# Kernel tuning notes

Hardware: AMD Instinct MI355X
Metric: run time of the kernel (lower is better)

The kernel has to match this reference:

```python
import jax, jax.numpy as jnp
import numpy as np

L, B, T = 512, 1024, 48

def setup_inputs() -> dict:
    key = jax.random.key(0)
    k0, k1, k2, k3, k4 = jax.random.split(key, 5)
    emissions = jax.random.normal(k0, (L, B, T), dtype=jnp.float32)
    tags = jax.random.randint(k1, (L, B), 0, T)
    mask = jnp.ones((L, B), dtype=jnp.int32)
    start_transitions = 0.1 * jax.random.normal(k2, (T,), dtype=jnp.float32)
    end_transitions = 0.1 * jax.random.normal(k3, (T,), dtype=jnp.float32)
    transitions = 0.1 * jax.random.normal(k4, (T, T), dtype=jnp.float32)
    return {"emissions": emissions, "tags": tags, "mask": mask,
            "start_transitions": start_transitions,
            "end_transitions": end_transitions,
            "transitions": transitions}


def _crf_llh(emissions, tags, mask, start_transitions, end_transitions, transitions):
    seq_len, batch, num_tags = emissions.shape
    maskf = mask.astype(emissions.dtype)

    # ---- numerator: joint log-likelihood of the gold tag path ----
    # emission score of the gold tag at each position: (L, B)
    emis_at_tags = jnp.take_along_axis(emissions, tags[:, :, None], axis=2)[:, :, 0]
    llh = start_transitions[tags[0]]                                  # (B,)
    llh = llh + jnp.sum(emis_at_tags[:-1] * maskf[:-1], axis=0)       # emissions for t=0..L-2
    trans_scores = transitions[tags[:-1], tags[1:]]                   # (L-1, B)
    llh = llh + jnp.sum(trans_scores * maskf[1:], axis=0)
    last_idx = jnp.sum(mask, axis=0).astype(jnp.int32) - 1            # (B,)
    last_tags = tags[last_idx, jnp.arange(batch)]                     # (B,)
    llh = llh + end_transitions[last_tags]
    llh = llh + emissions[-1][jnp.arange(batch), last_tags] * maskf[-1]

    # ---- denominator: log partition function via log-sum-exp scan ----
    def step(log_prob, x):
        e_t, m_t = x  # (B, T), (B,)
        # score[b, j] = logsumexp_i( log_prob[b, i] + trans[i, j] ) + e_t[b, j]
        score = jax.nn.logsumexp(log_prob[:, :, None] + transitions[None, :, :], axis=1) + e_t
        log_prob = jnp.where(m_t[:, None] > 0, score, log_prob)
        return log_prob, None

    init = start_transitions[None, :] + emissions[0]                  # (B, T)
    log_prob, _ = jax.lax.scan(step, init, (emissions[1:], maskf[1:]))
    log_z = jax.nn.logsumexp(log_prob + end_transitions[None, :], axis=1)  # (B,)

    return jnp.sum(llh - log_z)  # summed=True


def reference(emissions, tags, mask, start_transitions, end_transitions, transitions):
    return _crf_llh(emissions, tags, mask, start_transitions, end_transitions, transitions)
```

## Files before the change

kernel.cpp:

```cpp
#include <hip/hip_runtime.h>

#define Lq 512
#define Bn 1024
#define Tq 48

typedef float f32x4 __attribute__((ext_vector_type(4)));
typedef short s16x8 __attribute__((ext_vector_type(8)));
typedef unsigned u32x4 __attribute__((ext_vector_type(4)));

#define MFMA(a, b, c) __builtin_amdgcn_mfma_f32_16x16x32_bf16((a), (b), (c), 0, 0, 0)
#define SB __builtin_amdgcn_sched_barrier(0)

__device__ __forceinline__ unsigned cvtpk(float lo, float hi) {
    unsigned r;
    asm("v_cvt_pk_bf16_f32 %0, %1, %2" : "=v"(r) : "v"(lo), "v"(hi));
    return r;
}
__device__ __forceinline__ short f2b(float x) {
    unsigned u = __float_as_uint(x);
    return (short)((u + 0x7fffu + ((u >> 16) & 1u)) >> 16);
}

#define PACKB do {                                                            \
    unsigned d0_ = cvtpk(pn0[0], pn0[1]), d1_ = cvtpk(pn0[2], pn0[3]);        \
    unsigned d2_ = cvtpk(pn1[0], pn1[1]), d3_ = cvtpk(pn1[2], pn1[3]);        \
    unsigned d4_ = cvtpk(pn2[0], pn2[1]), d5_ = cvtpk(pn2[2], pn2[3]);        \
    u32x4 b0_ = {d0_, d1_, d2_, d3_};                                         \
    u32x4 b1_ = {d4_, d5_, 0u, 0u};                                           \
    Bk0 = __builtin_bit_cast(s16x8, b0_);                                     \
    Bk1 = __builtin_bit_cast(s16x8, b1_);                                     \
} while (0)

#define STEP(EA, EB, EC, MV, RS) do {                                         \
    f32x4 C0_ = MFMA(aw00, Bk0, Zf); f32x4 D0_ = MFMA(aw01, Bk1, Zf);         \
    f32x4 C1_ = MFMA(aw10, Bk0, Zf); f32x4 D1_ = MFMA(aw11, Bk1, Zf);         \
    f32x4 C2_ = MFMA(aw20, Bk0, Zf); f32x4 D2_ = MFMA(aw21, Bk1, Zf);         \
    pn0[0] = (MV) ? (C0_[0] + D0_[0]) * __expf((EA)[0]) : pn0[0];             \
    pn0[1] = (MV) ? (C0_[1] + D0_[1]) * __expf((EA)[1]) : pn0[1];             \
    pn0[2] = (MV) ? (C0_[2] + D0_[2]) * __expf((EA)[2]) : pn0[2];             \
    pn0[3] = (MV) ? (C0_[3] + D0_[3]) * __expf((EA)[3]) : pn0[3];             \
    pn1[0] = (MV) ? (C1_[0] + D1_[0]) * __expf((EB)[0]) : pn1[0];             \
    pn1[1] = (MV) ? (C1_[1] + D1_[1]) * __expf((EB)[1]) : pn1[1];             \
    pn1[2] = (MV) ? (C1_[2] + D1_[2]) * __expf((EB)[2]) : pn1[2];             \
    pn1[3] = (MV) ? (C1_[3] + D1_[3]) * __expf((EB)[3]) : pn1[3];             \
    pn2[0] = (MV) ? (C2_[0] + D2_[0]) * __expf((EC)[0]) : pn2[0];             \
    pn2[1] = (MV) ? (C2_[1] + D2_[1]) * __expf((EC)[1]) : pn2[1];             \
    pn2[2] = (MV) ? (C2_[2] + D2_[2]) * __expf((EC)[2]) : pn2[2];             \
    pn2[3] = (MV) ? (C2_[3] + D2_[3]) * __expf((EC)[3]) : pn2[3];             \
    if (RS) {                                                                 \
        float rep_ = __shfl(pn0[0], cidx, 64);         \
        int k_ = ((__float_as_int(rep_) >> 23) & 0xff) - 126;                 \
        float scl_ = __int_as_float((127 - k_) << 23);        \
        pn0[0]*=scl_; pn0[1]*=scl_; pn0[2]*=scl_; pn0[3]*=scl_;               \
        pn1[0]*=scl_; pn1[1]*=scl_; pn1[2]*=scl_; pn1[3]*=scl_;               \
        pn2[0]*=scl_; pn2[1]*=scl_; pn2[2]*=scl_; pn2[3]*=scl_;               \
        c2 += k_;                                                             \
    }                                                                         \
    PACKB;                                                                    \
} while (0)

#define LOAD_SLOT(D, T) do {                                                  \
    int t_ = (T); vf_##D = (t_ < Lq); int tc_ = vf_##D ? t_ : (Lq - 1);       \
    const float* ep_ = em + ((size_t)tc_ * Bn + bidx) * Tq + 4 * qidx;        \
    const int*   mp_ = mask + tc_ * Bn + bidx;                                \
    asm volatile("global_load_dwordx4 %0, %1, off" : "=v"(ea_##D) : "v"(ep_));      \
    asm volatile("global_load_dwordx4 %0, %1, off" : "=v"(eb_##D) : "v"(ep_ + 16)); \
    asm volatile("global_load_dwordx4 %0, %1, off" : "=v"(ec_##D) : "v"(ep_ + 32)); \
    asm volatile("global_load_dword %0, %1, off"   : "=v"(mv_##D) : "v"(mp_));      \
} while (0)

#define WAITP do { asm volatile("s_waitcnt vmcnt(12)"); SB; } while (0)

__global__ __launch_bounds__(64, 1) void crf_fused(
    const float* __restrict__ em, const int* __restrict__ tags,
    const int* __restrict__ mask, const float* __restrict__ startT,
    const float* __restrict__ endT, const float* __restrict__ trans,
    float* __restrict__ out)
{
    const int j = threadIdx.x;
    __shared__ float shf[Tq * Tq];

    if (blockIdx.x < 64) {
        const int cidx = j & 15;
        const int qidx = j >> 4;
        const int bidx = blockIdx.x * 16 + cidx;

        for (int i = j; i < Tq * Tq; i += 64) shf[i] = trans[i];
        __syncthreads();
        s16x8 aw00, aw01, aw10, aw11, aw20, aw21;
#pragma unroll
        for (int i = 0; i < 8; ++i) {
            int l0 = (i < 4) ? (4 * qidx + i) : (12 + 4 * qidx + i);
            aw00[i] = f2b(__expf(shf[l0 * Tq + cidx]));
            aw10[i] = f2b(__expf(shf[l0 * Tq + 16 + cidx]));
            aw20[i] = f2b(__expf(shf[l0 * Tq + 32 + cidx]));
            if (i < 4) {
                int l1 = 32 + 4 * qidx + i;
                aw01[i] = f2b(__expf(shf[l1 * Tq + cidx]));
                aw11[i] = f2b(__expf(shf[l1 * Tq + 16 + cidx]));
                aw21[i] = f2b(__expf(shf[l1 * Tq + 32 + cidx]));
            } else {
                aw01[i] = 0; aw11[i] = 0; aw21[i] = 0;
            }
        }

        f32x4 pn0, pn1, pn2;
        {
            const float* e0p = em + (size_t)bidx * Tq;
            f32x4 ea = *(const f32x4*)(e0p + 4 * qidx);
            f32x4 eb = *(const f32x4*)(e0p + 16 + 4 * qidx);
            f32x4 ec = *(const f32x4*)(e0p + 32 + 4 * qidx);
#pragma unroll
            for (int i = 0; i < 4; ++i) {
                pn0[i] = __expf(startT[ 0 + 4 * qidx + i] + ea[i]);
                pn1[i] = __expf(startT[16 + 4 * qidx + i] + eb[i]);
                pn2[i] = __expf(startT[32 + 4 * qidx + i] + ec[i]);
            }
        }

        const f32x4 Zf = {0.f, 0.f, 0.f, 0.f};
        s16x8 Bk0, Bk1;
        int c2 = 0;
        PACKB;

        f32x4 ea_0, eb_0, ec_0, ea_1, eb_1, ec_1;
        f32x4 ea_2, eb_2, ec_2, ea_3, eb_3, ec_3;
        int mv_0, mv_1, mv_2, mv_3;
        int vf_0, vf_1, vf_2, vf_3;

        asm volatile("s_waitcnt vmcnt(0)");
        LOAD_SLOT(0, 1); LOAD_SLOT(1, 2); LOAD_SLOT(2, 3); LOAD_SLOT(3, 4);

        for (int ch = 0; ch < 128; ++ch) {
            const int tb = 1 + 4 * ch;
            WAITP; STEP(ea_0, eb_0, ec_0, (mv_0 & vf_0), 0); LOAD_SLOT(0, tb + 4);
            WAITP; STEP(ea_1, eb_1, ec_1, (mv_1 & vf_1), 0); LOAD_SLOT(1, tb + 5);
            WAITP; STEP(ea_2, eb_2, ec_2, (mv_2 & vf_2), 0); LOAD_SLOT(2, tb + 6);
            WAITP; STEP(ea_3, eb_3, ec_3, (mv_3 & vf_3), 1); LOAD_SLOT(3, tb + 7);
        }

        float zacc = 0.f;
#pragma unroll
        for (int i = 0; i < 4; ++i) {
            zacc += pn0[i] * __expf(endT[ 0 + 4 * qidx + i]);
            zacc += pn1[i] * __expf(endT[16 + 4 * qidx + i]);
            zacc += pn2[i] * __expf(endT[32 + 4 * qidx + i]);
        }
        zacc += __shfl_xor(zacc, 16, 64);
        zacc += __shfl_xor(zacc, 32, 64);
        float nl = -(__logf(zacc) + (float)c2 * 0.6931471805599453f);
        nl += __shfl_xor(nl, 1, 64);
        nl += __shfl_xor(nl, 2, 64);
        nl += __shfl_xor(nl, 4, 64);
        nl += __shfl_xor(nl, 8, 64);
        if (j == 0) atomicAdd(out, nl);
        asm volatile("s_waitcnt vmcnt(0)");
    } else {
        const int bid = blockIdx.x - 64;
        float c = 0.0f;
        for (int id = bid * 64 + j; id < Lq * Bn; id += 512 * 64) {
            int t  = id >> 10;
            int bb = id & (Bn - 1);
            int tag = tags[id];
            int m_t = mask[id];
            if (t == 0) c += startT[tag];
            bool is_last;
            if (t < Lq - 1) {
                if (m_t) c += em[(size_t)id * Tq + tag];
                int tag1 = tags[id + Bn];
                int m1   = mask[id + Bn];
                if (m1) c += trans[tag * Tq + tag1];
                is_last = (m_t != 0) && (m1 == 0);
            } else {
                is_last = (m_t != 0);
            }
            if (is_last) {
                c += endT[tag];
                int mL = mask[(Lq - 1) * Bn + bb];
                if (mL) c += em[((size_t)(Lq - 1) * Bn + bb) * Tq + tag];
            }
        }
#pragma unroll
        for (int off = 32; off >= 1; off >>= 1)
            c += __shfl_xor(c, off, 64);
        if (j == 0) atomicAdd(out, c);
    }
}

extern "C" void kernel_launch(void* const* d_in, const int* in_sizes, int n_in,
                              void* d_out, int out_size, void* d_ws, size_t ws_size,
                              hipStream_t stream) {
    const float* em     = (const float*)d_in[0];
    const int*   tags   = (const int*)d_in[1];
    const int*   mask   = (const int*)d_in[2];
    const float* startT = (const float*)d_in[3];
    const float* endT   = (const float*)d_in[4];
    const float* trans  = (const float*)d_in[5];
    float* out = (float*)d_out;

    hipMemsetAsync(out, 0, sizeof(float), stream);
    crf_fused<<<576, 64, 0, stream>>>(em, tags, mask, startT, endT, trans, out);
}
```

Measured before the change: 150.6 us.

## Interleave two independent batch chains per wave to hide recurrence latency

Each forward-recursion wave now processes two 16-column batch groups (A and B) in an interleaved fashion, halving the recursion block count from 64 to 32. It also accumulates the two MFMA halves in place of separate adds, precomputes exp of emissions one slot ahead, and hoists the rescale exponent read before the rescale step. The intent is to fill the serial MFMA→exp→pack dependency chain with independent work from the second chain. In exchange, register pressure grows and fewer CUs are active for the latency-bound scan.

```diff
diff --git a/kernel.cpp b/kernel.cpp
--- a/kernel.cpp
+++ b/kernel.cpp
@@ -21,55 +21,73 @@
     return (short)((u + 0x7fffu + ((u >> 16) & 1u)) >> 16);
 }
 
-#define PACKB do {                                                            \
-    unsigned d0_ = cvtpk(pn0[0], pn0[1]), d1_ = cvtpk(pn0[2], pn0[3]);        \
-    unsigned d2_ = cvtpk(pn1[0], pn1[1]), d3_ = cvtpk(pn1[2], pn1[3]);        \
-    unsigned d4_ = cvtpk(pn2[0], pn2[1]), d5_ = cvtpk(pn2[2], pn2[3]);        \
+#define PACKBX(S) do {                                                        \
+    unsigned d0_ = cvtpk(pn##S##0[0], pn##S##0[1]);                           \
+    unsigned d1_ = cvtpk(pn##S##0[2], pn##S##0[3]);                           \
+    unsigned d2_ = cvtpk(pn##S##1[0], pn##S##1[1]);                           \
+    unsigned d3_ = cvtpk(pn##S##1[2], pn##S##1[3]);                           \
+    unsigned d4_ = cvtpk(pn##S##2[0], pn##S##2[1]);                           \
+    unsigned d5_ = cvtpk(pn##S##2[2], pn##S##2[3]);                           \
     u32x4 b0_ = {d0_, d1_, d2_, d3_};                                         \
     u32x4 b1_ = {d4_, d5_, 0u, 0u};                                           \
-    Bk0 = __builtin_bit_cast(s16x8, b0_);                                     \
-    Bk1 = __builtin_bit_cast(s16x8, b1_);                                     \
-} while (0)
-
-#define STEP(EA, EB, EC, MV, RS) do {                                         \
-    f32x4 C0_ = MFMA(aw00, Bk0, Zf); f32x4 D0_ = MFMA(aw01, Bk1, Zf);         \
-    f32x4 C1_ = MFMA(aw10, Bk0, Zf); f32x4 D1_ = MFMA(aw11, Bk1, Zf);         \
-    f32x4 C2_ = MFMA(aw20, Bk0, Zf); f32x4 D2_ = MFMA(aw21, Bk1, Zf);         \
-    pn0[0] = (MV) ? (C0_[0] + D0_[0]) * __expf((EA)[0]) : pn0[0];             \
-    pn0[1] = (MV) ? (C0_[1] + D0_[1]) * __expf((EA)[1]) : pn0[1];             \
-    pn0[2] = (MV) ? (C0_[2] + D0_[2]) * __expf((EA)[2]) : pn0[2];             \
-    pn0[3] = (MV) ? (C0_[3] + D0_[3]) * __expf((EA)[3]) : pn0[3];             \
-    pn1[0] = (MV) ? (C1_[0] + D1_[0]) * __expf((EB)[0]) : pn1[0];             \
-    pn1[1] = (MV) ? (C1_[1] + D1_[1]) * __expf((EB)[1]) : pn1[1];             \
-    pn1[2] = (MV) ? (C1_[2] + D1_[2]) * __expf((EB)[2]) : pn1[2];             \
-    pn1[3] = (MV) ? (C1_[3] + D1_[3]) * __expf((EB)[3]) : pn1[3];             \
-    pn2[0] = (MV) ? (C2_[0] + D2_[0]) * __expf((EC)[0]) : pn2[0];             \
-    pn2[1] = (MV) ? (C2_[1] + D2_[1]) * __expf((EC)[1]) : pn2[1];             \
-    pn2[2] = (MV) ? (C2_[2] + D2_[2]) * __expf((EC)[2]) : pn2[2];             \
-    pn2[3] = (MV) ? (C2_[3] + D2_[3]) * __expf((EC)[3]) : pn2[3];             \
+    Bk##S##0 = __builtin_bit_cast(s16x8, b0_);                                \
+    Bk##S##1 = __builtin_bit_cast(s16x8, b1_);                                \
+} while (0)
+
+#define STEPX(S, EA, EB, EC, MV, RS) do {                                     \
+    f32x4 C0_ = MFMA(aw00, Bk##S##0, Zf); C0_ = MFMA(aw01, Bk##S##1, C0_);    \
+    f32x4 C1_ = MFMA(aw10, Bk##S##0, Zf); C1_ = MFMA(aw11, Bk##S##1, C1_);    \
+    f32x4 C2_ = MFMA(aw20, Bk##S##0, Zf); C2_ = MFMA(aw21, Bk##S##1, C2_);    \
+    pn##S##0[0] = (MV) ? C0_[0] * (EA)[0] : pn##S##0[0];                      \
+    pn##S##0[1] = (MV) ? C0_[1] * (EA)[1] : pn##S##0[1];                      \
+    pn##S##0[2] = (MV) ? C0_[2] * (EA)[2] : pn##S##0[2];                      \
+    pn##S##0[3] = (MV) ? C0_[3] * (EA)[3] : pn##S##0[3];                      \
+    pn##S##1[0] = (MV) ? C1_[0] * (EB)[0] : pn##S##1[0];                      \
+    pn##S##1[1] = (MV) ? C1_[1] * (EB)[1] : pn##S##1[1];                      \
+    pn##S##1[2] = (MV) ? C1_[2] * (EB)[2] : pn##S##1[2];                      \
+    pn##S##1[3] = (MV) ? C1_[3] * (EB)[3] : pn##S##1[3];                      \
+    pn##S##2[0] = (MV) ? C2_[0] * (EC)[0] : pn##S##2[0];                      \
+    pn##S##2[1] = (MV) ? C2_[1] * (EC)[1] : pn##S##2[1];                      \
+    pn##S##2[2] = (MV) ? C2_[2] * (EC)[2] : pn##S##2[2];                      \
+    pn##S##2[3] = (MV) ? C2_[3] * (EC)[3] : pn##S##2[3];                      \
     if (RS) {                                                                 \
-        float rep_ = __shfl(pn0[0], cidx, 64);         \
-        int k_ = ((__float_as_int(rep_) >> 23) & 0xff) - 126;                 \
-        float scl_ = __int_as_float((127 - k_) << 23);        \
-        pn0[0]*=scl_; pn0[1]*=scl_; pn0[2]*=scl_; pn0[3]*=scl_;               \
-        pn1[0]*=scl_; pn1[1]*=scl_; pn1[2]*=scl_; pn1[3]*=scl_;               \
-        pn2[0]*=scl_; pn2[1]*=scl_; pn2[2]*=scl_; pn2[3]*=scl_;               \
-        c2 += k_;                                                             \
+        pn##S##0[0]*=scl##S; pn##S##0[1]*=scl##S;                             \
+        pn##S##0[2]*=scl##S; pn##S##0[3]*=scl##S;                             \
+        pn##S##1[0]*=scl##S; pn##S##1[1]*=scl##S;                             \
+        pn##S##1[2]*=scl##S; pn##S##1[3]*=scl##S;                             \
+        pn##S##2[0]*=scl##S; pn##S##2[1]*=scl##S;                             \
+        pn##S##2[2]*=scl##S; pn##S##2[3]*=scl##S;                             \
+        c2##S += k##S;                                                        \
     }                                                                         \
-    PACKB;                                                                    \
-} while (0)
-
-#define LOAD_SLOT(D, T) do {                                                  \
-    int t_ = (T); vf_##D = (t_ < Lq); int tc_ = vf_##D ? t_ : (Lq - 1);       \
-    const float* ep_ = em + ((size_t)tc_ * Bn + bidx) * Tq + 4 * qidx;        \
-    const int*   mp_ = mask + tc_ * Bn + bidx;                                \
-    asm volatile("global_load_dwordx4 %0, %1, off" : "=v"(ea_##D) : "v"(ep_));      \
-    asm volatile("global_load_dwordx4 %0, %1, off" : "=v"(eb_##D) : "v"(ep_ + 16)); \
-    asm volatile("global_load_dwordx4 %0, %1, off" : "=v"(ec_##D) : "v"(ep_ + 32)); \
-    asm volatile("global_load_dword %0, %1, off"   : "=v"(mv_##D) : "v"(mp_));      \
-} while (0)
-
-#define WAITP do { asm volatile("s_waitcnt vmcnt(12)"); SB; } while (0)
+    PACKBX(S);                                                                \
+} while (0)
+
+#define KREADX(S) do {                                                        \
+    float rep_ = __shfl(pn##S##0[0], cidx, 64);                               \
+    k##S = ((__float_as_int(rep_) >> 23) & 0xff) - 126;                       \
+    scl##S = __int_as_float((127 - k##S) << 23);                              \
+} while (0)
+
+#define LOAD_SLOTX(S, D, T) do {                                              \
+    int t_ = (T); vf##S##_##D = (t_ < Lq); int tc_ = vf##S##_##D ? t_ : (Lq - 1); \
+    const float* ep_ = em + ((size_t)tc_ * Bn + bidx##S) * Tq + 4 * qidx;     \
+    const int*   mp_ = mask + tc_ * Bn + bidx##S;                             \
+    asm volatile("global_load_dwordx4 %0, %1, off" : "=v"(ea##S##_##D) : "v"(ep_));      \
+    asm volatile("global_load_dwordx4 %0, %1, off" : "=v"(eb##S##_##D) : "v"(ep_ + 16)); \
+    asm volatile("global_load_dwordx4 %0, %1, off" : "=v"(ec##S##_##D) : "v"(ep_ + 32)); \
+    asm volatile("global_load_dword %0, %1, off"   : "=v"(mv##S##_##D) : "v"(mp_));      \
+} while (0)
+
+#define EXP_SLOTX(S, D) do {                                                  \
+    ea##S##_##D[0]=__expf(ea##S##_##D[0]); ea##S##_##D[1]=__expf(ea##S##_##D[1]); \
+    ea##S##_##D[2]=__expf(ea##S##_##D[2]); ea##S##_##D[3]=__expf(ea##S##_##D[3]); \
+    eb##S##_##D[0]=__expf(eb##S##_##D[0]); eb##S##_##D[1]=__expf(eb##S##_##D[1]); \
+    eb##S##_##D[2]=__expf(eb##S##_##D[2]); eb##S##_##D[3]=__expf(eb##S##_##D[3]); \
+    ec##S##_##D[0]=__expf(ec##S##_##D[0]); ec##S##_##D[1]=__expf(ec##S##_##D[1]); \
+    ec##S##_##D[2]=__expf(ec##S##_##D[2]); ec##S##_##D[3]=__expf(ec##S##_##D[3]); \
+} while (0)
+
+#define WAIT16 do { asm volatile("s_waitcnt vmcnt(16)"); SB; } while (0)
 
 __global__ __launch_bounds__(64, 1) void crf_fused(
     const float* __restrict__ em, const int* __restrict__ tags,
@@ -80,10 +98,11 @@
     const int j = threadIdx.x;
     __shared__ float shf[Tq * Tq];
 
-    if (blockIdx.x < 64) {
+    if (blockIdx.x < 32) {
         const int cidx = j & 15;
         const int qidx = j >> 4;
-        const int bidx = blockIdx.x * 16 + cidx;
+        const int bidxA = blockIdx.x * 32 + cidx;
+        const int bidxB = bidxA + 16;
 
         for (int i = j; i < Tq * Tq; i += 64) shf[i] = trans[i];
         __syncthreads();
@@ -104,51 +123,90 @@
             }
         }
 
-        f32x4 pn0, pn1, pn2;
-        {
-            const float* e0p = em + (size_t)bidx * Tq;
+        f32x4 pnA0, pnA1, pnA2, pnB0, pnB1, pnB2;
+#pragma unroll
+        for (int s = 0; s < 2; ++s) {
+            const float* e0p = em + (size_t)(s ? bidxB : bidxA) * Tq;
             f32x4 ea = *(const f32x4*)(e0p + 4 * qidx);
             f32x4 eb = *(const f32x4*)(e0p + 16 + 4 * qidx);
             f32x4 ec = *(const f32x4*)(e0p + 32 + 4 * qidx);
+            f32x4 p0, p1, p2;
 #pragma unroll
             for (int i = 0; i < 4; ++i) {
-                pn0[i] = __expf(startT[ 0 + 4 * qidx + i] + ea[i]);
-                pn1[i] = __expf(startT[16 + 4 * qidx + i] + eb[i]);
-                pn2[i] = __expf(startT[32 + 4 * qidx + i] + ec[i]);
-            }
+                p0[i] = __expf(startT[ 0 + 4 * qidx + i] + ea[i]);
+                p1[i] = __expf(startT[16 + 4 * qidx + i] + eb[i]);
+                p2[i] = __expf(startT[32 + 4 * qidx + i] + ec[i]);
+            }
+            if (s) { pnB0 = p0; pnB1 = p1; pnB2 = p2; }
+            else   { pnA0 = p0; pnA1 = p1; pnA2 = p2; }
         }
 
         const f32x4 Zf = {0.f, 0.f, 0.f, 0.f};
-        s16x8 Bk0, Bk1;
-        int c2 = 0;
-        PACKB;
-
-        f32x4 ea_0, eb_0, ec_0, ea_1, eb_1, ec_1;
-        f32x4 ea_2, eb_2, ec_2, ea_3, eb_3, ec_3;
-        int mv_0, mv_1, mv_2, mv_3;
-        int vf_0, vf_1, vf_2, vf_3;
+        s16x8 BkA0, BkA1, BkB0, BkB1;
+        int c2A = 0, c2B = 0;
+        int kA = 0, kB = 0;
+        float sclA = 1.0f, sclB = 1.0f;
+        PACKBX(A); PACKBX(B);
+
+        f32x4 eaA_0, ebA_0, ecA_0, eaA_1, ebA_1, ecA_1;
+        f32x4 eaA_2, ebA_2, ecA_2, eaA_3, ebA_3, ecA_3;
+        f32x4 eaB_0, ebB_0, ecB_0, eaB_1, ebB_1, ecB_1;
+        f32x4 eaB_2, ebB_2, ecB_2, eaB_3, ebB_3, ecB_3;
+        int mvA_0, mvA_1, mvA_2, mvA_3, mvB_0, mvB_1, mvB_2, mvB_3;
+        int vfA_0, vfA_1, vfA_2, vfA_3, vfB_0, vfB_1, vfB_2, vfB_3;
 
         asm volatile("s_waitcnt vmcnt(0)");
-        LOAD_SLOT(0, 1); LOAD_SLOT(1, 2); LOAD_SLOT(2, 3); LOAD_SLOT(3, 4);
+        LOAD_SLOTX(A, 0, 1); LOAD_SLOTX(B, 0, 1);
+        LOAD_SLOTX(A, 1, 2); LOAD_SLOTX(B, 1, 2);
+        LOAD_SLOTX(A, 2, 3); LOAD_SLOTX(B, 2, 3);
+        LOAD_SLOTX(A, 3, 4); LOAD_SLOTX(B, 3, 4);
+        WAIT16;
+        EXP_SLOTX(A, 0); EXP_SLOTX(B, 0);
 
         for (int ch = 0; ch < 128; ++ch) {
             const int tb = 1 + 4 * ch;
-            WAITP; STEP(ea_0, eb_0, ec_0, (mv_0 & vf_0), 0); LOAD_SLOT(0, tb + 4);
-            WAITP; STEP(ea_1, eb_1, ec_1, (mv_1 & vf_1), 0); LOAD_SLOT(1, tb + 5);
-            WAITP; STEP(ea_2, eb_2, ec_2, (mv_2 & vf_2), 0); LOAD_SLOT(2, tb + 6);
-            WAITP; STEP(ea_3, eb_3, ec_3, (mv_3 & vf_3), 1); LOAD_SLOT(3, tb + 7);
-        }
-
-        float zacc = 0.f;
+            WAIT16;
+            EXP_SLOTX(A, 1); EXP_SLOTX(B, 1);
+            STEPX(A, eaA_0, ebA_0, ecA_0, (mvA_0 & vfA_0), 0);
+            STEPX(B, eaB_0, ebB_0, ecB_0, (mvB_0 & vfB_0), 0);
+            LOAD_SLOTX(A, 0, tb + 4); LOAD_SLOTX(B, 0, tb + 4);
+
+            WAIT16;
+            EXP_SLOTX(A, 2); EXP_SLOTX(B, 2);
+            STEPX(A, eaA_1, ebA_1, ecA_1, (mvA_1 & vfA_1), 0);
+            STEPX(B, eaB_1, ebB_1, ecB_1, (mvB_1 & vfB_1), 0);
+            LOAD_SLOTX(A, 1, tb + 5); LOAD_SLOTX(B, 1, tb + 5);
+
+            WAIT16;
+            EXP_SLOTX(A, 3); EXP_SLOTX(B, 3);
+            STEPX(A, eaA_2, ebA_2, ecA_2, (mvA_2 & vfA_2), 0); KREADX(A);
+            STEPX(B, eaB_2, ebB_2, ecB_2, (mvB_2 & vfB_2), 0); KREADX(B);
+            LOAD_SLOTX(A, 2, tb + 6); LOAD_SLOTX(B, 2, tb + 6);
+
+            WAIT16;
+            EXP_SLOTX(A, 0); EXP_SLOTX(B, 0);
+            STEPX(A, eaA_3, ebA_3, ecA_3, (mvA_3 & vfA_3), 1);
+            STEPX(B, eaB_3, ebB_3, ecB_3, (mvB_3 & vfB_3), 1);
+            LOAD_SLOTX(A, 3, tb + 7); LOAD_SLOTX(B, 3, tb + 7);
+        }
+
+        float ezq0[4], ezq1[4], ezq2[4];
 #pragma unroll
         for (int i = 0; i < 4; ++i) {
-            zacc += pn0[i] * __expf(endT[ 0 + 4 * qidx + i]);
-            zacc += pn1[i] * __expf(endT[16 + 4 * qidx + i]);
-            zacc += pn2[i] * __expf(endT[32 + 4 * qidx + i]);
-        }
-        zacc += __shfl_xor(zacc, 16, 64);
-        zacc += __shfl_xor(zacc, 32, 64);
-        float nl = -(__logf(zacc) + (float)c2 * 0.6931471805599453f);
+            ezq0[i] = __expf(endT[ 0 + 4 * qidx + i]);
+            ezq1[i] = __expf(endT[16 + 4 * qidx + i]);
+            ezq2[i] = __expf(endT[32 + 4 * qidx + i]);
+        }
+        float zA = 0.f, zB = 0.f;
+#pragma unroll
+        for (int i = 0; i < 4; ++i) {
+            zA += pnA0[i] * ezq0[i] + pnA1[i] * ezq1[i] + pnA2[i] * ezq2[i];
+            zB += pnB0[i] * ezq0[i] + pnB1[i] * ezq1[i] + pnB2[i] * ezq2[i];
+        }
+        zA += __shfl_xor(zA, 16, 64); zA += __shfl_xor(zA, 32, 64);
+        zB += __shfl_xor(zB, 16, 64); zB += __shfl_xor(zB, 32, 64);
+        float nl = -(__logf(zA) + (float)c2A * 0.6931471805599453f)
+                 - (__logf(zB) + (float)c2B * 0.6931471805599453f);
         nl += __shfl_xor(nl, 1, 64);
         nl += __shfl_xor(nl, 2, 64);
         nl += __shfl_xor(nl, 4, 64);
@@ -156,7 +214,7 @@
         if (j == 0) atomicAdd(out, nl);
         asm volatile("s_waitcnt vmcnt(0)");
     } else {
-        const int bid = blockIdx.x - 64;
+        const int bid = blockIdx.x - 32;
         float c = 0.0f;
         for (int id = bid * 64 + j; id < Lq * Bn; id += 512 * 64) {
             int t  = id >> 10;
@@ -199,5 +257,5 @@
     float* out = (float*)d_out;
 
     hipMemsetAsync(out, 0, sizeof(float), stream);
-    crf_fused<<<576, 64, 0, stream>>>(em, tags, mask, startT, endT, trans, out);
-}
+    crf_fused<<<544, 64, 0, stream>>>(em, tags, mask, startT, endT, trans, out);
+}
```

After: 223.3 us. 48.3% more time.
